# Kernel tuning notes

Hardware: AMD Instinct MI355X
Metric: run time of the kernel (lower is better)

The kernel has to match this reference:

```python
import jax, jax.numpy as jnp
import numpy as np

N_NODES = 100000
N_EDGES = 1600000
IN_CH, HID_CH, OUT_CH = 128, 128, 40


def setup_inputs() -> dict:
    key = jax.random.key(0)
    ks = jax.random.split(key, 7)
    s = 1.0 / np.sqrt(IN_CH)
    s2 = 1.0 / np.sqrt(HID_CH)
    return {
        "x": jax.random.normal(ks[0], (N_NODES, IN_CH), jnp.float32),
        "edge_index": jax.random.randint(ks[1], (2, N_EDGES), 0, N_NODES, jnp.int64),
        "W1l": jax.random.normal(ks[2], (IN_CH, HID_CH), jnp.float32) * s,
        "b1": jnp.zeros((HID_CH,), jnp.float32),
        "W1r": jax.random.normal(ks[3], (IN_CH, HID_CH), jnp.float32) * s,
        "W2l": jax.random.normal(ks[4], (HID_CH, OUT_CH), jnp.float32) * s2,
        "b2": jnp.zeros((OUT_CH,), jnp.float32),
        "W2r": jax.random.normal(ks[5], (HID_CH, OUT_CH), jnp.float32) * s2,
    }


def reference(x, edge_index, W1l, b1, W1r, W2l, b2, W2r):
    src, dst = edge_index[0], edge_index[1]
    # per-target in-degree for mean aggregation (zero-degree nodes -> 0 output)
    deg = jax.ops.segment_sum(jnp.ones((src.shape[0],), x.dtype), dst,
                              num_segments=N_NODES)
    inv_deg = jnp.where(deg > 0, 1.0 / jnp.maximum(deg, 1.0), 0.0)[:, None]

    def sage(h, Wl, b, Wr):
        # gather source features, scatter-sum to targets, normalize -> mean
        agg = jax.ops.segment_sum(h[src], dst, num_segments=N_NODES) * inv_deg
        return agg @ Wl + b + h @ Wr

    h = jax.nn.relu(sage(x, W1l, b1, W1r))
    # F.dropout(p=0.5) defaults to training=True -> active dropout
    keep = jax.random.bernoulli(jax.random.key(42), 0.5, h.shape)
    h = jnp.where(keep, h * 2.0, 0.0)
    out = sage(h, W2l, b2, W2r)
    return jax.nn.log_softmax(out, axis=1)
```

## Files before the change

kernel.cpp:

```cpp
#include <hip/hip_runtime.h>
#include <stdint.h>
#include <stddef.h>

#define N_NODES 100000
#define N_EDGES 1600000
#define IN_CH 128
#define HID_CH 128
#define OUT_CH 40

#define NB 196
#define GCAP 10240
#define TILE_EDGES 2048
#define LCAP 40

#define N_MASK_WORDS 400000
#define N_CVT4 3200000

#define WROW 264

typedef __attribute__((ext_vector_type(8))) short bf16x8;
typedef __attribute__((ext_vector_type(8))) unsigned short u16x8;
typedef __attribute__((ext_vector_type(4))) float f32x4;

__device__ __forceinline__ ushort f2bf(float f) {
    uint32_t u = __float_as_uint(f);
    uint32_t r = (u + 0x7FFFu + ((u >> 16) & 1u)) >> 16;
    return (ushort)r;
}
__device__ __forceinline__ float bf2f(ushort u) {
    return __uint_as_float(((uint32_t)u) << 16);
}

__device__ __forceinline__ uint32_t rotl32(uint32_t x, int r) {
    return (x << r) | (x >> (32 - r));
}

__device__ __forceinline__ void threefry2x32_k42(uint32_t x0, uint32_t x1,
                                                 uint32_t& o0, uint32_t& o1) {
    const uint32_t ks0 = 0u, ks1 = 42u;
    const uint32_t ks2 = 0u ^ 42u ^ 0x1BD11BDAu;
    x0 += ks0; x1 += ks1;
    x0 += x1; x1 = rotl32(x1, 13); x1 ^= x0;
    x0 += x1; x1 = rotl32(x1, 15); x1 ^= x0;
    x0 += x1; x1 = rotl32(x1, 26); x1 ^= x0;
    x0 += x1; x1 = rotl32(x1,  6); x1 ^= x0;
    x0 += ks1; x1 += ks2 + 1u;
    x0 += x1; x1 = rotl32(x1, 17); x1 ^= x0;
    x0 += x1; x1 = rotl32(x1, 29); x1 ^= x0;
    x0 += x1; x1 = rotl32(x1, 16); x1 ^= x0;
    x0 += x1; x1 = rotl32(x1, 24); x1 ^= x0;
    x0 += ks2; x1 += ks0 + 2u;
    x0 += x1; x1 = rotl32(x1, 13); x1 ^= x0;
    x0 += x1; x1 = rotl32(x1, 15); x1 ^= x0;
    x0 += x1; x1 = rotl32(x1, 26); x1 ^= x0;
    x0 += x1; x1 = rotl32(x1,  6); x1 ^= x0;
    x0 += ks0; x1 += ks1 + 3u;
    x0 += x1; x1 = rotl32(x1, 17); x1 ^= x0;
    x0 += x1; x1 = rotl32(x1, 29); x1 ^= x0;
    x0 += x1; x1 = rotl32(x1, 16); x1 ^= x0;
    x0 += x1; x1 = rotl32(x1, 24); x1 ^= x0;
    x0 += ks1; x1 += ks2 + 4u;
    x0 += x1; x1 = rotl32(x1, 13); x1 ^= x0;
    x0 += x1; x1 = rotl32(x1, 15); x1 ^= x0;
    x0 += x1; x1 = rotl32(x1, 26); x1 ^= x0;
    x0 += x1; x1 = rotl32(x1,  6); x1 ^= x0;
    x0 += ks2; x1 += ks0 + 5u;
    o0 = x0; o1 = x1;
}

__device__ __forceinline__ void load_edge(const void* ei, bool is32, int e,
                                          int& s, int& d) {
    if (is32) {
        const int* p = (const int*)ei;
        s = p[e]; d = p[N_EDGES + e];
    } else {
        const long long* p = (const long long*)ei;
        s = (int)p[e]; d = (int)p[N_EDGES + e];
    }
}

__global__ __launch_bounds__(256) void prep(const int* __restrict__ ei32,
                                            int* __restrict__ flag,
                                            int* __restrict__ gcnt) {
    const int t = threadIdx.x;
    if (blockIdx.x == 0) {
        __shared__ int red[256];
        int local = 0;
        #pragma unroll
        for (int j = 0; j < 64; ++j) {
            int k = (t * 64 + j) * 97;
            local |= ei32[2 * k + 1];
        }
        red[t] = local;
        __syncthreads();
        for (int off = 128; off; off >>= 1) {
            if (t < off) red[t] |= red[t + off];
            __syncthreads();
        }
        if (t == 0) *flag = (red[0] != 0);
    } else {
        for (int i = t; i < NB * 16; i += 256) gcnt[i] = 0;
    }
}

__global__ __launch_bounds__(256) void bucket_edges(
    const void* __restrict__ ei, const int* __restrict__ flag,
    int* __restrict__ gcnt, uint2* __restrict__ gbuf) {
    __shared__ uint2 lbuf[NB][LCAP];
    __shared__ int lcnt[NB];
    const bool is32 = (*flag != 0);
    const int t = threadIdx.x;
    for (int b = t; b < NB; b += 256) lcnt[b] = 0;
    __syncthreads();
    const int base = blockIdx.x * TILE_EDGES;
    #pragma unroll
    for (int j = 0; j < TILE_EDGES / 256; ++j) {
        int e = base + j * 256 + t;
        if (e < N_EDGES) {
            int s, d;
            load_edge(ei, is32, e, s, d);
            int b = d >> 9;
            int pos = atomicAdd(&lcnt[b], 1);
            if (pos < LCAP) {
                lbuf[b][pos] = make_uint2((uint32_t)s, (uint32_t)d);
            } else {
                int gp = atomicAdd(&gcnt[b * 16], 1);
                gbuf[(size_t)b * GCAP + gp] = make_uint2((uint32_t)s, (uint32_t)d);
            }
        }
    }
    __syncthreads();
    if (t < NB) {
        int cnt = lcnt[t];
        if (cnt > LCAP) cnt = LCAP;
        if (cnt > 0) {
            int gp = atomicAdd(&gcnt[t * 16], cnt);
            uint2* dst = gbuf + (size_t)t * GCAP + gp;
            for (int i = 0; i < cnt; ++i) dst[i] = lbuf[t][i];
        }
    }
}

__global__ void bucket_scan(const int* __restrict__ gcnt, int* __restrict__ bbase) {
    __shared__ int s[256];
    int t = threadIdx.x;
    int tot = (t < NB) ? gcnt[t * 16] : 0;
    s[t] = tot;
    __syncthreads();
    for (int off = 1; off < 256; off <<= 1) {
        int a = (t >= off) ? s[t - off] : 0;
        __syncthreads();
        s[t] += a;
        __syncthreads();
    }
    if (t < NB) bbase[t] = s[t] - tot;
}

__global__ __launch_bounds__(256) void build_csr(
    const int* __restrict__ gcnt, const uint2* __restrict__ gbuf,
    const int* __restrict__ bbase, int* __restrict__ csr, int* __restrict__ cursor) {
    __shared__ int hist[512];
    __shared__ int excl[512];
    __shared__ int cur[512];
    __shared__ int psum[256];
    const int b = blockIdx.x;
    const int t = threadIdx.x;
    hist[t] = 0; hist[t + 256] = 0;
    __syncthreads();
    const int base = bbase[b];
    const int cnt = gcnt[b * 16];
    const uint2* src = gbuf + (size_t)b * GCAP;
    for (int i = t; i < cnt; i += 256)
        atomicAdd(&hist[src[i].y & 511], 1);
    __syncthreads();
    int h0 = hist[2 * t], h1 = hist[2 * t + 1];
    psum[t] = h0 + h1;
    __syncthreads();
    int v = psum[t];
    for (int off = 1; off < 256; off <<= 1) {
        int a = (t >= off) ? psum[t - off] : 0;
        __syncthreads();
        psum[t] += a;
        __syncthreads();
    }
    int pex = psum[t] - v;
    excl[2 * t] = pex;
    excl[2 * t + 1] = pex + h0;
    cur[2 * t] = pex;
    cur[2 * t + 1] = pex + h0;
    __syncthreads();
    for (int j = t; j < 512; j += 256) {
        int node = b * 512 + j;
        if (node < N_NODES) cursor[node] = base + excl[j] + hist[j];
    }
    for (int i = t; i < cnt; i += 256) {
        uint2 p = src[i];
        int pos = atomicAdd(&cur[p.y & 511], 1);
        csr[base + pos] = (int)p.x;
    }
}

__global__ __launch_bounds__(256) void cvt_and_mask(
    const float* __restrict__ in, ushort* __restrict__ out,
    uint32_t* __restrict__ mask) {
    const long gid = (long)blockIdx.x * blockDim.x + threadIdx.x;
    const long stride = (long)gridDim.x * blockDim.x;
    for (long i = gid; i < N_CVT4; i += stride) {
        float4 v = *reinterpret_cast<const float4*>(in + i * 4);
        ushort4 r;
        r.x = f2bf(v.x); r.y = f2bf(v.y); r.z = f2bf(v.z); r.w = f2bf(v.w);
        *reinterpret_cast<ushort4*>(out + i * 4) = r;
    }
    for (long w = gid; w < N_MASK_WORDS; w += stride) {
        uint32_t m = 0;
        #pragma unroll 4
        for (int j = 0; j < 32; ++j) {
            uint32_t o0, o1;
            threefry2x32_k42(0u, (uint32_t)w * 32u + j, o0, o1);
            m |= ((o0 ^ o1) >> 31) << j;
        }
        mask[w] = m;
    }
}

__global__ void cvt_w2(const float* __restrict__ W1l, const float* __restrict__ W1r,
                       const float* __restrict__ W2l, const float* __restrict__ W2r,
                       ushort* __restrict__ Wt1, ushort* __restrict__ Wt2) {
    int blk = blockIdx.x;
    int k = threadIdx.x;
    if (blk < 128) {
        int n = blk;
        float v = (k < 128) ? W1l[(size_t)k * 128 + n] : W1r[(size_t)(k - 128) * 128 + n];
        Wt1[(size_t)n * 256 + k] = f2bf(v);
    } else {
        int n = blk - 128;
        float v = 0.0f;
        if (n < OUT_CH)
            v = (k < 128) ? W2l[(size_t)k * 40 + n] : W2r[(size_t)(k - 128) * 40 + n];
        Wt2[(size_t)n * 256 + k] = f2bf(v);
    }
}

__global__ __launch_bounds__(256) void aggregate_mean_bf(
    const ushort* __restrict__ feat, const int* __restrict__ csr,
    const int* __restrict__ cursor, ushort* __restrict__ out) {
    int node = blockIdx.x * 4 + (threadIdx.x >> 6);
    if (node >= N_NODES) return;
    const int lane = threadIdx.x & 63;
    const int g = lane >> 4;
    const int c = lane & 15;
    const int beg = (node > 0) ? cursor[node - 1] : 0;
    const int end = cursor[node];
    const int deg = end - beg;

    int myidx = (lane < deg) ? csr[beg + lane] : 0;

    float acc[8];
    #pragma unroll
    for (int j = 0; j < 8; ++j) acc[j] = 0.0f;

    const int nfull = (deg < 64) ? deg : 64;
    const int niter = (nfull + 3) >> 2;
    #pragma unroll 4
    for (int k = 0; k < niter; ++k) {
        int e = g + 4 * k;
        bool valid = (e < nfull);
        int es = valid ? e : 0;
        int s = __shfl(myidx, es, 64);
        float w = valid ? 1.0f : 0.0f;
        bf16x8 v = *reinterpret_cast<const bf16x8*>(feat + (size_t)s * 128 + c * 8);
        #pragma unroll
        for (int j = 0; j < 8; ++j) acc[j] += w * bf2f((ushort)v[j]);
    }
    for (int e = 64 + g; e < deg; e += 4) {
        int s = csr[beg + e];
        bf16x8 v = *reinterpret_cast<const bf16x8*>(feat + (size_t)s * 128 + c * 8);
        #pragma unroll
        for (int j = 0; j < 8; ++j) acc[j] += bf2f((ushort)v[j]);
    }

    #pragma unroll
    for (int j = 0; j < 8; ++j) {
        acc[j] += __shfl_xor(acc[j], 16, 64);
        acc[j] += __shfl_xor(acc[j], 32, 64);
    }

    if (g == 0) {
        float inv = (deg > 0) ? (1.0f / (float)deg) : 0.0f;
        u16x8 r;
        #pragma unroll
        for (int j = 0; j < 8; ++j) r[j] = f2bf(acc[j] * inv);
        *reinterpret_cast<u16x8*>(out + (size_t)node * 128 + c * 8) = r;
    }
}

__global__ __launch_bounds__(256) void layer1_mfma(
    const ushort* __restrict__ agg, const ushort* __restrict__ xbf,
    const ushort* __restrict__ Wt, const float* __restrict__ b1,
    const uint32_t* __restrict__ dmask, ushort* __restrict__ h) {
    __shared__ ushort wlds[64 * WROW];
    const int tid = threadIdx.x;
    const int lane = tid & 63;
    const int l15 = lane & 15, kg = lane >> 4;
    const int colBase = (blockIdx.x & 1) * 64;
    const int row_base = ((blockIdx.x >> 1) * 4 + (tid >> 6)) * 16;

    #pragma unroll
    for (int i = 0; i < 8; ++i) {
        int idx = tid + i * 256;
        int r = idx >> 5, c = idx & 31;
        u16x8 v = *reinterpret_cast<const u16x8*>(Wt + (size_t)(colBase + r) * 256 + c * 8);
        *reinterpret_cast<u16x8*>(wlds + r * WROW + c * 8) = v;
    }
    __syncthreads();
    if (row_base >= N_NODES) return;

    int r0 = row_base + l15;
    int r0c = (r0 < N_NODES) ? r0 : (N_NODES - 1);

    bf16x8 a[8];
    #pragma unroll
    for (int ks = 0; ks < 4; ++ks) {
        a[ks]     = *reinterpret_cast<const bf16x8*>(agg + (size_t)r0c * 128 + ks * 32 + kg * 8);
        a[ks + 4] = *reinterpret_cast<const bf16x8*>(xbf + (size_t)r0c * 128 + ks * 32 + kg * 8);
    }

    f32x4 acc[4];
    #pragma unroll
    for (int nf = 0; nf < 4; ++nf) acc[nf] = (f32x4){0.f, 0.f, 0.f, 0.f};

    #pragma unroll
    for (int nf = 0; nf < 4; ++nf) {
        const ushort* bp = wlds + (nf * 16 + l15) * WROW + kg * 8;
        #pragma unroll
        for (int ks = 0; ks < 8; ++ks) {
            bf16x8 b = *reinterpret_cast<const bf16x8*>(bp + ks * 32);
            acc[nf] = __builtin_amdgcn_mfma_f32_16x16x32_bf16(a[ks], b, acc[nf], 0, 0, 0);
        }
    }

    #pragma unroll
    for (int r = 0; r < 4; ++r) {
        int row = row_base + kg * 4 + r;
        if (row < N_NODES) {
            uint4 mw = *reinterpret_cast<const uint4*>(dmask + (size_t)row * 4);
            const uint32_t* mwp = reinterpret_cast<const uint32_t*>(&mw);
            #pragma unroll
            for (int nf = 0; nf < 4; ++nf) {
                int col = colBase + nf * 16 + l15;
                float v = acc[nf][r] + b1[col];
                v = fmaxf(v, 0.0f) * 2.0f;
                if ((mwp[col >> 5] >> (col & 31)) & 1u) v = 0.0f;
                h[(size_t)row * 128 + col] = f2bf(v);
            }
        }
    }
}

__global__ __launch_bounds__(256) void layer2_mfma(
    const ushort* __restrict__ agg, const ushort* __restrict__ hbf,
    const ushort* __restrict__ Wt2, const float* __restrict__ b2,
    float* __restrict__ out) {
    __shared__ ushort wlds[48 * WROW];
    const int tid = threadIdx.x;
    const int lane = tid & 63;
    const int l15 = lane & 15, kg = lane >> 4;
    const int row_base = (blockIdx.x * 4 + (tid >> 6)) * 16;

    #pragma unroll
    for (int i = 0; i < 6; ++i) {
        int idx = tid + i * 256;
        int r = idx >> 5, c = idx & 31;
        u16x8 v = *reinterpret_cast<const u16x8*>(Wt2 + (size_t)r * 256 + c * 8);
        *reinterpret_cast<u16x8*>(wlds + r * WROW + c * 8) = v;
    }
    __syncthreads();
    if (row_base >= N_NODES) return;

    int r0 = row_base + l15;
    int r0c = (r0 < N_NODES) ? r0 : (N_NODES - 1);

    bf16x8 a[8];
    #pragma unroll
    for (int ks = 0; ks < 4; ++ks) {
        a[ks]     = *reinterpret_cast<const bf16x8*>(agg + (size_t)r0c * 128 + ks * 32 + kg * 8);
        a[ks + 4] = *reinterpret_cast<const bf16x8*>(hbf + (size_t)r0c * 128 + ks * 32 + kg * 8);
    }

    f32x4 acc[3];
    #pragma unroll
    for (int nf = 0; nf < 3; ++nf) acc[nf] = (f32x4){0.f, 0.f, 0.f, 0.f};

    #pragma unroll
    for (int nf = 0; nf < 3; ++nf) {
        const ushort* bp = wlds + (nf * 16 + l15) * WROW + kg * 8;
        #pragma unroll
        for (int ks = 0; ks < 8; ++ks) {
            bf16x8 b = *reinterpret_cast<const bf16x8*>(bp + ks * 32);
            acc[nf] = __builtin_amdgcn_mfma_f32_16x16x32_bf16(a[ks], b, acc[nf], 0, 0, 0);
        }
    }

    #pragma unroll
    for (int r = 0; r < 4; ++r) {
        int row = row_base + kg * 4 + r;
        float v[3];
        #pragma unroll
        for (int nf = 0; nf < 3; ++nf) {
            int col = nf * 16 + l15;
            v[nf] = (col < OUT_CH) ? (acc[nf][r] + b2[col]) : -3.0e38f;
        }
        float mx = fmaxf(fmaxf(v[0], v[1]), v[2]);
        #pragma unroll
        for (int s = 1; s < 16; s <<= 1) mx = fmaxf(mx, __shfl_xor(mx, s, 64));
        float se = 0.0f;
        #pragma unroll
        for (int nf = 0; nf < 3; ++nf) {
            int col = nf * 16 + l15;
            if (col < OUT_CH) se += expf(v[nf] - mx);
        }
        #pragma unroll
        for (int s = 1; s < 16; s <<= 1) se += __shfl_xor(se, s, 64);
        float lz = mx + logf(se);
        if (row < N_NODES) {
            #pragma unroll
            for (int nf = 0; nf < 3; ++nf) {
                int col = nf * 16 + l15;
                if (col < OUT_CH)
                    out[(size_t)row * OUT_CH + col] = v[nf] - lz;
            }
        }
    }
}

extern "C" void kernel_launch(void* const* d_in, const int* in_sizes, int n_in,
                              void* d_out, int out_size, void* d_ws, size_t ws_size,
                              hipStream_t stream) {
    const float* x   = (const float*)d_in[0];
    const void*  ei  = d_in[1];
    const float* W1l = (const float*)d_in[2];
    const float* b1  = (const float*)d_in[3];
    const float* W1r = (const float*)d_in[4];
    const float* W2l = (const float*)d_in[5];
    const float* b2  = (const float*)d_in[6];
    const float* W2r = (const float*)d_in[7];
    float* out = (float*)d_out;

    char* ws = (char*)d_ws;
    int*      flag   = (int*)ws;
    int*      gcnt   = (int*)(ws + 4096);
    int*      bbase  = (int*)(ws + 106496);
    ushort*   x_bf   = (ushort*)(ws + 131072);
    ushort*   h_bf   = (ushort*)(ws + 131072 + 25600000);
    ushort*   agg_bf = (ushort*)(ws + 131072 + 51200000);
    ushort*   Wt1    = (ushort*)(ws + 131072 + 76800000);
    ushort*   Wt2    = (ushort*)(ws + 131072 + 76865536);
    uint2*    gbuf   = (uint2*)(ws + 77021184);
    uint32_t* dmask  = (uint32_t*)(ws + 93077504);

    char* ob = (char*)d_out;
    int* csr    = (int*)ob;
    int* cursor = (int*)(ob + 6400000);

    prep<<<2, 256, 0, stream>>>((const int*)ei, flag, gcnt);
    bucket_edges<<<(N_EDGES + TILE_EDGES - 1) / TILE_EDGES, 256, 0, stream>>>(
        ei, flag, gcnt, gbuf);
    bucket_scan<<<1, 256, 0, stream>>>(gcnt, bbase);
    build_csr<<<NB, 256, 0, stream>>>(gcnt, gbuf, bbase, csr, cursor);

    cvt_and_mask<<<2048, 256, 0, stream>>>(x, x_bf, dmask);
    cvt_w2<<<176, 256, 0, stream>>>(W1l, W1r, W2l, W2r, Wt1, Wt2);

    aggregate_mean_bf<<<(N_NODES + 3) / 4, 256, 0, stream>>>(x_bf, csr, cursor, agg_bf);
    layer1_mfma<<<2 * ((N_NODES + 63) / 64), 256, 0, stream>>>(agg_bf, x_bf, Wt1, b1, dmask, h_bf);
    aggregate_mean_bf<<<(N_NODES + 3) / 4, 256, 0, stream>>>(h_bf, csr, cursor, agg_bf);
    layer2_mfma<<<(N_NODES + 63) / 64, 256, 0, stream>>>(agg_bf, h_bf, Wt2, b2, out);
}
```

Baseline: 293.0 us.

## Apply layer-2 weights before aggregation to gather 40-wide features instead of 128

Layer 2 is reordered so h is first multiplied by [W2l|W2r] into an 80-wide bf16 product. Only the 40-wide W2l half is then mean-aggregated over neighbors, and a separate kernel adds the root term and bias and applies log_softmax. This uses linearity of mean aggregation to cut second-layer gather traffic from 128 to 40 channels per edge. In exchange it adds an extra kernel launch and an intermediate buffer, with bf16 rounding of pre-aggregation products.

New measurement: 271.7 us. -7.3%, faster.

```diff
diff --git a/kernel.cpp b/kernel.cpp
--- a/kernel.cpp
+++ b/kernel.cpp
@@ -17,6 +17,7 @@
 #define N_CVT4 3200000
 
 #define WROW 264
+#define WROW2 136
 
 typedef __attribute__((ext_vector_type(8))) short bf16x8;
 typedef __attribute__((ext_vector_type(8))) unsigned short u16x8;
@@ -232,12 +233,11 @@
         int n = blk;
         float v = (k < 128) ? W1l[(size_t)k * 128 + n] : W1r[(size_t)(k - 128) * 128 + n];
         Wt1[(size_t)n * 256 + k] = f2bf(v);
-    } else {
+    } else if (k < 128) {
         int n = blk - 128;
-        float v = 0.0f;
-        if (n < OUT_CH)
-            v = (k < 128) ? W2l[(size_t)k * 40 + n] : W2r[(size_t)(k - 128) * 40 + n];
-        Wt2[(size_t)n * 256 + k] = f2bf(v);
+        float v = (n < OUT_CH) ? W2l[(size_t)k * 40 + n]
+                               : W2r[(size_t)k * 40 + (n - OUT_CH)];
+        Wt2[(size_t)n * 128 + k] = f2bf(v);
     }
 }
 
@@ -357,22 +357,21 @@
     }
 }
 
-__global__ __launch_bounds__(256) void layer2_mfma(
-    const ushort* __restrict__ agg, const ushort* __restrict__ hbf,
-    const ushort* __restrict__ Wt2, const float* __restrict__ b2,
-    float* __restrict__ out) {
-    __shared__ ushort wlds[48 * WROW];
+__global__ __launch_bounds__(256) void layer2_pre(
+    const ushort* __restrict__ hbf, const ushort* __restrict__ Wt2,
+    ushort* __restrict__ y2z2) {
+    __shared__ ushort wlds[80 * WROW2];
     const int tid = threadIdx.x;
     const int lane = tid & 63;
     const int l15 = lane & 15, kg = lane >> 4;
     const int row_base = (blockIdx.x * 4 + (tid >> 6)) * 16;
 
     #pragma unroll
-    for (int i = 0; i < 6; ++i) {
+    for (int i = 0; i < 5; ++i) {
         int idx = tid + i * 256;
-        int r = idx >> 5, c = idx & 31;
-        u16x8 v = *reinterpret_cast<const u16x8*>(Wt2 + (size_t)r * 256 + c * 8);
-        *reinterpret_cast<u16x8*>(wlds + r * WROW + c * 8) = v;
+        int r = idx >> 4, c = idx & 15;
+        u16x8 v = *reinterpret_cast<const u16x8*>(Wt2 + (size_t)r * 128 + c * 8);
+        *reinterpret_cast<u16x8*>(wlds + r * WROW2 + c * 8) = v;
     }
     __syncthreads();
     if (row_base >= N_NODES) return;
@@ -380,22 +379,20 @@
     int r0 = row_base + l15;
     int r0c = (r0 < N_NODES) ? r0 : (N_NODES - 1);
 
-    bf16x8 a[8];
-    #pragma unroll
-    for (int ks = 0; ks < 4; ++ks) {
-        a[ks]     = *reinterpret_cast<const bf16x8*>(agg + (size_t)r0c * 128 + ks * 32 + kg * 8);
-        a[ks + 4] = *reinterpret_cast<const bf16x8*>(hbf + (size_t)r0c * 128 + ks * 32 + kg * 8);
-    }
-
-    f32x4 acc[3];
-    #pragma unroll
-    for (int nf = 0; nf < 3; ++nf) acc[nf] = (f32x4){0.f, 0.f, 0.f, 0.f};
-
-    #pragma unroll
-    for (int nf = 0; nf < 3; ++nf) {
-        const ushort* bp = wlds + (nf * 16 + l15) * WROW + kg * 8;
-        #pragma unroll
-        for (int ks = 0; ks < 8; ++ks) {
+    bf16x8 a[4];
+    #pragma unroll
+    for (int ks = 0; ks < 4; ++ks)
+        a[ks] = *reinterpret_cast<const bf16x8*>(hbf + (size_t)r0c * 128 + ks * 32 + kg * 8);
+
+    f32x4 acc[5];
+    #pragma unroll
+    for (int nf = 0; nf < 5; ++nf) acc[nf] = (f32x4){0.f, 0.f, 0.f, 0.f};
+
+    #pragma unroll
+    for (int nf = 0; nf < 5; ++nf) {
+        const ushort* bp = wlds + (nf * 16 + l15) * WROW2 + kg * 8;
+        #pragma unroll
+        for (int ks = 0; ks < 4; ++ks) {
             bf16x8 b = *reinterpret_cast<const bf16x8*>(bp + ks * 32);
             acc[nf] = __builtin_amdgcn_mfma_f32_16x16x32_bf16(a[ks], b, acc[nf], 0, 0, 0);
         }
@@ -404,32 +401,101 @@
     #pragma unroll
     for (int r = 0; r < 4; ++r) {
         int row = row_base + kg * 4 + r;
-        float v[3];
-        #pragma unroll
-        for (int nf = 0; nf < 3; ++nf) {
-            int col = nf * 16 + l15;
-            v[nf] = (col < OUT_CH) ? (acc[nf][r] + b2[col]) : -3.0e38f;
-        }
-        float mx = fmaxf(fmaxf(v[0], v[1]), v[2]);
-        #pragma unroll
-        for (int s = 1; s < 16; s <<= 1) mx = fmaxf(mx, __shfl_xor(mx, s, 64));
-        float se = 0.0f;
-        #pragma unroll
-        for (int nf = 0; nf < 3; ++nf) {
-            int col = nf * 16 + l15;
-            if (col < OUT_CH) se += expf(v[nf] - mx);
-        }
-        #pragma unroll
-        for (int s = 1; s < 16; s <<= 1) se += __shfl_xor(se, s, 64);
-        float lz = mx + logf(se);
         if (row < N_NODES) {
             #pragma unroll
-            for (int nf = 0; nf < 3; ++nf) {
+            for (int nf = 0; nf < 5; ++nf) {
                 int col = nf * 16 + l15;
-                if (col < OUT_CH)
-                    out[(size_t)row * OUT_CH + col] = v[nf] - lz;
+                y2z2[(size_t)row * 80 + col] = f2bf(acc[nf][r]);
             }
         }
+    }
+}
+
+__global__ __launch_bounds__(256) void aggregate_mean_40(
+    const ushort* __restrict__ y2, const int* __restrict__ csr,
+    const int* __restrict__ cursor, ushort* __restrict__ aggy2) {
+    int node = blockIdx.x * 4 + (threadIdx.x >> 6);
+    if (node >= N_NODES) return;
+    const int lane = threadIdx.x & 63;
+    const int g = lane >> 3;
+    const int c = lane & 7;
+    const int cc = (c < 5) ? c : (c - 5);
+    const float cw = (c < 5) ? 1.0f : 0.0f;
+    const int beg = (node > 0) ? cursor[node - 1] : 0;
+    const int end = cursor[node];
+    const int deg = end - beg;
+
+    int myidx = (lane < deg) ? csr[beg + lane] : 0;
+
+    float acc[8];
+    #pragma unroll
+    for (int j = 0; j < 8; ++j) acc[j] = 0.0f;
+
+    const int nfull = (deg < 64) ? deg : 64;
+    const int niter = (nfull + 7) >> 3;
+    for (int k = 0; k < niter; ++k) {
+        int e = g + 8 * k;
+        bool valid = (e < nfull);
+        int es = valid ? e : 0;
+        int s = __shfl(myidx, es, 64);
+        float w = valid ? cw : 0.0f;
+        bf16x8 v = *reinterpret_cast<const bf16x8*>(y2 + (size_t)s * 80 + cc * 8);
+        #pragma unroll
+        for (int j = 0; j < 8; ++j) acc[j] += w * bf2f((ushort)v[j]);
+    }
+    for (int e = 64 + g; e < deg; e += 8) {
+        int s = csr[beg + e];
+        bf16x8 v = *reinterpret_cast<const bf16x8*>(y2 + (size_t)s * 80 + cc * 8);
+        #pragma unroll
+        for (int j = 0; j < 8; ++j) acc[j] += cw * bf2f((ushort)v[j]);
+    }
+
+    #pragma unroll
+    for (int j = 0; j < 8; ++j) {
+        acc[j] += __shfl_xor(acc[j], 8, 64);
+        acc[j] += __shfl_xor(acc[j], 16, 64);
+        acc[j] += __shfl_xor(acc[j], 32, 64);
+    }
+
+    if (lane < 5) {
+        float inv = (deg > 0) ? (1.0f / (float)deg) : 0.0f;
+        u16x8 r;
+        #pragma unroll
+        for (int j = 0; j < 8; ++j) r[j] = f2bf(acc[j] * inv);
+        *reinterpret_cast<u16x8*>(aggy2 + (size_t)node * 40 + lane * 8) = r;
+    }
+}
+
+__global__ __launch_bounds__(256) void layer2_post(
+    const ushort* __restrict__ aggy2, const ushort* __restrict__ y2z2,
+    const float* __restrict__ b2, float* __restrict__ out) {
+    int node = blockIdx.x * blockDim.x + threadIdx.x;
+    if (node >= N_NODES) return;
+
+    float v[40];
+    #pragma unroll
+    for (int i = 0; i < 5; ++i) {
+        u16x8 av = *reinterpret_cast<const u16x8*>(aggy2 + (size_t)node * 40 + i * 8);
+        u16x8 zv = *reinterpret_cast<const u16x8*>(y2z2 + (size_t)node * 80 + 40 + i * 8);
+        #pragma unroll
+        for (int j = 0; j < 8; ++j)
+            v[i * 8 + j] = bf2f((ushort)av[j]) + bf2f((ushort)zv[j]) + b2[i * 8 + j];
+    }
+    float mx = -1e30f;
+    #pragma unroll
+    for (int j = 0; j < 40; ++j) mx = fmaxf(mx, v[j]);
+    float se = 0.0f;
+    #pragma unroll
+    for (int j = 0; j < 40; ++j) se += expf(v[j] - mx);
+    float lz = mx + logf(se);
+    #pragma unroll
+    for (int i = 0; i < 10; ++i) {
+        float4 r;
+        r.x = v[i * 4 + 0] - lz;
+        r.y = v[i * 4 + 1] - lz;
+        r.z = v[i * 4 + 2] - lz;
+        r.w = v[i * 4 + 3] - lz;
+        *reinterpret_cast<float4*>(out + (size_t)node * 40 + i * 4) = r;
     }
 }
 
@@ -458,6 +524,9 @@
     uint2*    gbuf   = (uint2*)(ws + 77021184);
     uint32_t* dmask  = (uint32_t*)(ws + 93077504);
 
+    ushort* y2z2  = (ushort*)(ws + 131072 + 51200000);
+    ushort* aggy2 = (ushort*)(ws + 131072 + 51200000 + 16000000);
+
     char* ob = (char*)d_out;
     int* csr    = (int*)ob;
     int* cursor = (int*)(ob + 6400000);
@@ -469,10 +538,12 @@
     build_csr<<<NB, 256, 0, stream>>>(gcnt, gbuf, bbase, csr, cursor);
 
     cvt_and_mask<<<2048, 256, 0, stream>>>(x, x_bf, dmask);
-    cvt_w2<<<176, 256, 0, stream>>>(W1l, W1r, W2l, W2r, Wt1, Wt2);
+    cvt_w2<<<208, 256, 0, stream>>>(W1l, W1r, W2l, W2r, Wt1, Wt2);
 
     aggregate_mean_bf<<<(N_NODES + 3) / 4, 256, 0, stream>>>(x_bf, csr, cursor, agg_bf);
     layer1_mfma<<<2 * ((N_NODES + 63) / 64), 256, 0, stream>>>(agg_bf, x_bf, Wt1, b1, dmask, h_bf);
-    aggregate_mean_bf<<<(N_NODES + 3) / 4, 256, 0, stream>>>(h_bf, csr, cursor, agg_bf);
-    layer2_mfma<<<(N_NODES + 63) / 64, 256, 0, stream>>>(agg_bf, h_bf, Wt2, b2, out);
-}
+
+    layer2_pre<<<(N_NODES + 63) / 64, 256, 0, stream>>>(h_bf, Wt2, y2z2);
+    aggregate_mean_40<<<(N_NODES + 3) / 4, 256, 0, stream>>>(y2z2, csr, cursor, aggy2);
+    layer2_post<<<(N_NODES + 255) / 256, 256, 0, stream>>>(aggy2, y2z2, b2, out);
+}
```
